# Optimization experiments

Hardware: AMD Instinct MI355X
Metric: run time of the kernel (lower is better)

The kernel has to match this reference:

```python
import jax, jax.numpy as jnp
import numpy as np

# Decode-mode paged attention: equivalent math to the Pallas paged_attention kernel
# the module dispatches to. Shapes per PagedAttentionOp init args.
B, H, D = 32, 32, 128        # decode batch, query heads, head dim
KVH = 8                      # num_kv_heads (GQA group = H // KVH = 4)
P, T = 2048, 64              # num_pages (global pool), tokens_per_page
PPS = 64                     # pages per sequence (page_map width)
MAXLEN = PPS * T             # 4096 max context


def setup_inputs() -> dict:
    key = jax.random.key(0)
    k1, k2, k3, k4, k5 = jax.random.split(key, 5)
    q = jax.random.normal(k1, (B, H, D), jnp.float32)
    k_pages = jax.random.normal(k2, (KVH, P, T, D), jnp.float32)
    v_pages = jax.random.normal(k3, (KVH, P, T, D), jnp.float32)
    lengths = jnp.maximum(jax.random.randint(k4, (B,), 0, MAXLEN), 1).astype(jnp.int32)
    page_indices = jax.random.randint(k5, (B, PPS), 0, P).astype(jnp.int32)
    return {"q": q, "k_pages": k_pages, "v_pages": v_pages,
            "lengths": lengths, "page_indices": page_indices}


def reference(q, k_pages, v_pages, lengths, page_indices):
    # q: [B, H, D]; k_pages/v_pages: [KVH, P, T, D]
    # lengths: [B] valid token counts; page_indices: [B, PPS] page table
    kvh, _, t, d = k_pages.shape
    b, h, _ = q.shape
    g = h // kvh                      # GQA group size
    s = page_indices.shape[1] * t     # gathered context length
    # page-table gather: [KVH, B, PPS, T, D] -> [KVH, B, S, D]
    k = jnp.take(k_pages, page_indices, axis=1).reshape(kvh, b, s, d)
    v = jnp.take(v_pages, page_indices, axis=1).reshape(kvh, b, s, d)
    qr = q.reshape(b, kvh, g, d)
    # no 1/sqrt(d) scaling: module never scales (MaxText pre-scales queries)
    scores = jnp.einsum('bkgd,kbsd->bkgs', qr, k)  # [B, KVH, G, S]
    valid = jnp.arange(s, dtype=jnp.int32)[None, :] < lengths[:, None]  # [B, S]
    scores = jnp.where(valid[:, None, None, :], scores, jnp.float32(-1e10))
    probs = jax.nn.softmax(scores, axis=-1)
    out = jnp.einsum('bkgs,kbsd->bkgd', probs, v)  # [B, KVH, G, D]
    return out.reshape(b, h, d)
```

## Files before the change

### kernel.cpp

```cpp
#include <hip/hip_runtime.h>
#include <math.h>

#define B_    32
#define H_    32
#define D_    128
#define KVH_  8
#define G_    4
#define P_    2048
#define T_    64
#define PPS_  64
#define NCHUNK 8
#define CHUNK_PAGES 8
#define RS4   33

__global__ __launch_bounds__(256, 2)
void pa_partial(const float* __restrict__ q,
                const float* __restrict__ k_pages,
                const float* __restrict__ v_pages,
                const int*   __restrict__ lengths,
                const int*   __restrict__ page_indices,
                float* __restrict__ o_part,
                float* __restrict__ m_part,
                float* __restrict__ l_part)
{
    __shared__ float4 K4[T_ * RS4];
    __shared__ float4 V4[T_ * RS4];
    __shared__ float4 q4s[G_ * 32];
    __shared__ float  p_s[G_ * T_];
    __shared__ float  alpha_s[G_];

    const int tid = threadIdx.x;
    const int bx  = blockIdx.x;
    const int c   = bx & (NCHUNK - 1);
    const int k   = (bx >> 3) & (KVH_ - 1);
    const int b   = bx >> 6;

    const int len = lengths[b];
    const int chunk_tok0 = c * (CHUNK_PAGES * T_);
    if (chunk_tok0 >= len) return;

    const int nP = (len + T_ - 1) / T_;
    const int p0 = c * CHUNK_PAGES;
    const int p1 = min(nP, p0 + CHUNK_PAGES);

    {
        const float* qg = q + ((size_t)b * H_ + (size_t)k * G_) * D_;
        ((float*)q4s)[tid]       = qg[tid];
        ((float*)q4s)[tid + 256] = qg[tid + 256];
    }

    const int g = tid >> 6;
    const int t = tid & 63;
    float m_run = -INFINITY;
    float l_run = 0.f;

    const int dq = tid & 31;
    const int th = tid >> 5;
    float4 oacc[G_];
#pragma unroll
    for (int i = 0; i < G_; ++i) { oacc[i].x = 0.f; oacc[i].y = 0.f; oacc[i].z = 0.f; oacc[i].w = 0.f; }

    __syncthreads();

    for (int p = p0; p < p1; ++p) {
        const int page = page_indices[b * PPS_ + p];
        const float4* Kg = (const float4*)(k_pages + ((size_t)k * P_ + (size_t)page) * (T_ * D_));
        const float4* Vg = (const float4*)(v_pages + ((size_t)k * P_ + (size_t)page) * (T_ * D_));

#pragma unroll
        for (int i = 0; i < 8; ++i) {
            const int f  = tid + 256 * i;
            const int tt = f >> 5;
            const int jj = f & 31;
            K4[tt * RS4 + jj] = Kg[f];
            V4[tt * RS4 + jj] = Vg[f];
        }
        __syncthreads();

        float s = 0.f;
        {
            const float4* Kr = &K4[t * RS4];
            const float4* qr = &q4s[g * 32];
#pragma unroll
            for (int i = 0; i < 32; ++i) {
                const float4 kv = Kr[i];
                const float4 qv = qr[i];
                s += kv.x * qv.x + kv.y * qv.y + kv.z * qv.z + kv.w * qv.w;
            }
        }
        const int tok = p * T_ + t;
        if (tok >= len) s = -1e30f;

        float smax = s;
#pragma unroll
        for (int off = 32; off; off >>= 1) smax = fmaxf(smax, __shfl_xor(smax, off));
        const float m_new = fmaxf(m_run, smax);
        const float pr    = __expf(s - m_new);
        const float alpha = __expf(m_run - m_new);
        float psum = pr;
#pragma unroll
        for (int off = 32; off; off >>= 1) psum += __shfl_xor(psum, off);
        l_run = alpha * l_run + psum;
        m_run = m_new;
        p_s[g * T_ + t] = pr;
        if (t == 0) alpha_s[g] = alpha;
        __syncthreads();

        const float a0 = alpha_s[0], a1 = alpha_s[1], a2 = alpha_s[2], a3 = alpha_s[3];
        oacc[0].x *= a0; oacc[0].y *= a0; oacc[0].z *= a0; oacc[0].w *= a0;
        oacc[1].x *= a1; oacc[1].y *= a1; oacc[1].z *= a1; oacc[1].w *= a1;
        oacc[2].x *= a2; oacc[2].y *= a2; oacc[2].z *= a2; oacc[2].w *= a2;
        oacc[3].x *= a3; oacc[3].y *= a3; oacc[3].z *= a3; oacc[3].w *= a3;
#pragma unroll
        for (int tt = 0; tt < 8; ++tt) {
            const int t2 = th * 8 + tt;
            const float4 vv = V4[t2 * RS4 + dq];
            const float pv0 = p_s[0 * T_ + t2];
            const float pv1 = p_s[1 * T_ + t2];
            const float pv2 = p_s[2 * T_ + t2];
            const float pv3 = p_s[3 * T_ + t2];
            oacc[0].x += pv0 * vv.x; oacc[0].y += pv0 * vv.y; oacc[0].z += pv0 * vv.z; oacc[0].w += pv0 * vv.w;
            oacc[1].x += pv1 * vv.x; oacc[1].y += pv1 * vv.y; oacc[1].z += pv1 * vv.z; oacc[1].w += pv1 * vv.w;
            oacc[2].x += pv2 * vv.x; oacc[2].y += pv2 * vv.y; oacc[2].z += pv2 * vv.z; oacc[2].w += pv2 * vv.w;
            oacc[3].x += pv3 * vv.x; oacc[3].y += pv3 * vv.y; oacc[3].z += pv3 * vv.z; oacc[3].w += pv3 * vv.w;
        }
        __syncthreads();
    }

    float4* red = K4;
#pragma unroll
    for (int g2 = 0; g2 < G_; ++g2) red[(th * G_ + g2) * 32 + dq] = oacc[g2];
    if (t == 0) { m_part[bx * G_ + g] = m_run; l_part[bx * G_ + g] = l_run; }
    __syncthreads();

    if (tid < 128) {
        const int gg = tid >> 5;
        const int dd = tid & 31;
        float4 sum; sum.x = 0.f; sum.y = 0.f; sum.z = 0.f; sum.w = 0.f;
#pragma unroll
        for (int th2 = 0; th2 < 8; ++th2) {
            const float4 v = red[(th2 * G_ + gg) * 32 + dd];
            sum.x += v.x; sum.y += v.y; sum.z += v.z; sum.w += v.w;
        }
        float4* op = (float4*)(o_part + (size_t)bx * (G_ * D_));
        op[gg * 32 + dd] = sum;
    }
}

__global__ __launch_bounds__(128)
void pa_reduce(const float* __restrict__ o_part,
               const float* __restrict__ m_part,
               const float* __restrict__ l_part,
               const int*   __restrict__ lengths,
               float* __restrict__ out)
{
    const int bx = blockIdx.x;
    const int gg = bx & 3;
    const int k  = (bx >> 2) & 7;
    const int b  = bx >> 5;
    const int len = lengths[b];
    const int nc  = (len + 511) >> 9;
    const int base = (b * KVH_ + k) * NCHUNK;

    float M = -INFINITY;
#pragma unroll
    for (int c = 0; c < NCHUNK; ++c)
        if (c < nc) M = fmaxf(M, m_part[(base + c) * G_ + gg]);

    const int d = threadIdx.x;
    float L = 0.f;
    float acc = 0.f;
#pragma unroll
    for (int c = 0; c < NCHUNK; ++c) {
        if (c < nc) {
            const float wc = __expf(m_part[(base + c) * G_ + gg] - M);
            L   += wc * l_part[(base + c) * G_ + gg];
            acc += wc * o_part[(size_t)(base + c) * (G_ * D_) + gg * D_ + d];
        }
    }
    out[((size_t)b * H_ + (size_t)k * G_ + gg) * D_ + d] = acc / L;
}

extern "C" void kernel_launch(void* const* d_in, const int* in_sizes, int n_in,
                              void* d_out, int out_size, void* d_ws, size_t ws_size,
                              hipStream_t stream) {
    const float* q            = (const float*)d_in[0];
    const float* k_pages      = (const float*)d_in[1];
    const float* v_pages      = (const float*)d_in[2];
    const int*   lengths      = (const int*)d_in[3];
    const int*   page_indices = (const int*)d_in[4];
    float* out = (float*)d_out;

    float* o_part = (float*)d_ws;
    float* m_part = o_part + (size_t)2048 * (G_ * D_);
    float* l_part = m_part + (size_t)2048 * G_;

    pa_partial<<<B_ * KVH_ * NCHUNK, 256, 0, stream>>>(
        q, k_pages, v_pages, lengths, page_indices, o_part, m_part, l_part);
    pa_reduce<<<B_ * KVH_ * G_, 128, 0, stream>>>(
        o_part, m_part, l_part, lengths, out);
}
```

Measured before the change: 922.0 us.

## Prefetch K pages via direct global-to-LDS loads, stream V through registers

K tiles are now staged asynchronously into LDS with global_load_lds and an XOR swizzle in place of padding, and the next page is prefetched while the current PV product runs. V is loaded straight into registers instead of going through shared memory, which halves LDS use and allows four blocks per CU. The split-K chunking doubles to 16 chunks of 4 pages for more parallelism, at the cost of more partial results to reduce. This relies on correct vmcnt handling at the barriers for the async LDS loads.

```diff
diff --git a/kernel.cpp b/kernel.cpp
--- a/kernel.cpp
+++ b/kernel.cpp
@@ -9,11 +9,16 @@
 #define P_    2048
 #define T_    64
 #define PPS_  64
-#define NCHUNK 8
-#define CHUNK_PAGES 8
-#define RS4   33
-
-__global__ __launch_bounds__(256, 2)
+#define NCHUNK 16
+#define CHUNK_PAGES 4
+
+__device__ __forceinline__ void load_lds16(const float4* g, void* l) {
+    __builtin_amdgcn_global_load_lds(
+        (const __attribute__((address_space(1))) void*)g,
+        (__attribute__((address_space(3))) void*)l, 16, 0, 0);
+}
+
+__global__ __launch_bounds__(256, 4)
 void pa_partial(const float* __restrict__ q,
                 const float* __restrict__ k_pages,
                 const float* __restrict__ v_pages,
@@ -23,8 +28,7 @@
                 float* __restrict__ m_part,
                 float* __restrict__ l_part)
 {
-    __shared__ float4 K4[T_ * RS4];
-    __shared__ float4 V4[T_ * RS4];
+    __shared__ float4 K4s[T_ * 32];
     __shared__ float4 q4s[G_ * 32];
     __shared__ float  p_s[G_ * T_];
     __shared__ float  alpha_s[G_];
@@ -32,14 +36,13 @@
     const int tid = threadIdx.x;
     const int bx  = blockIdx.x;
     const int c   = bx & (NCHUNK - 1);
-    const int k   = (bx >> 3) & (KVH_ - 1);
-    const int b   = bx >> 6;
+    const int k   = (bx >> 4) & (KVH_ - 1);
+    const int b   = bx >> 7;
 
     const int len = lengths[b];
-    const int chunk_tok0 = c * (CHUNK_PAGES * T_);
-    if (chunk_tok0 >= len) return;
-
-    const int nP = (len + T_ - 1) / T_;
+    if (c * (CHUNK_PAGES * T_) >= len) return;
+
+    const int nP = (len + T_ - 1) >> 6;
     const int p0 = c * CHUNK_PAGES;
     const int p1 = min(nP, p0 + CHUNK_PAGES);
 
@@ -49,46 +52,52 @@
         ((float*)q4s)[tid + 256] = qg[tid + 256];
     }
 
-    const int g = tid >> 6;
-    const int t = tid & 63;
+    const int g  = tid >> 6;
+    const int t  = tid & 63;
+    const int dq = tid & 31;
+    const int th = tid >> 5;
+
+    const int* pt = page_indices + b * PPS_;
+
     float m_run = -INFINITY;
     float l_run = 0.f;
-
-    const int dq = tid & 31;
-    const int th = tid >> 5;
     float4 oacc[G_];
 #pragma unroll
     for (int i = 0; i < G_; ++i) { oacc[i].x = 0.f; oacc[i].y = 0.f; oacc[i].z = 0.f; oacc[i].w = 0.f; }
 
-    __syncthreads();
+    auto stageK = [&](const float4* Kg) {
+#pragma unroll
+        for (int i = 0; i < 8; ++i) {
+            const int Lb = (g * 8 + i) * 64;
+            const int t_ = (Lb >> 5) + (t >> 5);
+            const int j_ = (t & 31) ^ (t_ & 7);
+            load_lds16(Kg + t_ * 32 + j_, (void*)&K4s[Lb]);
+        }
+    };
+
+    stageK((const float4*)(k_pages + ((size_t)k * P_ + pt[p0]) * (T_ * D_)));
 
     for (int p = p0; p < p1; ++p) {
-        const int page = page_indices[b * PPS_ + p];
-        const float4* Kg = (const float4*)(k_pages + ((size_t)k * P_ + (size_t)page) * (T_ * D_));
-        const float4* Vg = (const float4*)(v_pages + ((size_t)k * P_ + (size_t)page) * (T_ * D_));
-
-#pragma unroll
-        for (int i = 0; i < 8; ++i) {
-            const int f  = tid + 256 * i;
-            const int tt = f >> 5;
-            const int jj = f & 31;
-            K4[tt * RS4 + jj] = Kg[f];
-            V4[tt * RS4 + jj] = Vg[f];
-        }
         __syncthreads();
+
+        const float4* Vg = (const float4*)(v_pages + ((size_t)k * P_ + pt[p]) * (T_ * D_));
+        float4 vv[8];
+#pragma unroll
+        for (int tt = 0; tt < 8; ++tt) vv[tt] = Vg[(th * 8 + tt) * 32 + dq];
 
         float s = 0.f;
         {
-            const float4* Kr = &K4[t * RS4];
+            const float4* Kr = &K4s[t * 32];
             const float4* qr = &q4s[g * 32];
+            const int sw = t & 7;
 #pragma unroll
             for (int i = 0; i < 32; ++i) {
-                const float4 kv = Kr[i];
+                const float4 kv = Kr[i ^ sw];
                 const float4 qv = qr[i];
                 s += kv.x * qv.x + kv.y * qv.y + kv.z * qv.z + kv.w * qv.w;
             }
         }
-        const int tok = p * T_ + t;
+        const int tok = (p << 6) + t;
         if (tok >= len) s = -1e30f;
 
         float smax = s;
@@ -102,9 +111,12 @@
         for (int off = 32; off; off >>= 1) psum += __shfl_xor(psum, off);
         l_run = alpha * l_run + psum;
         m_run = m_new;
-        p_s[g * T_ + t] = pr;
+        p_s[(g << 6) + t] = pr;
         if (t == 0) alpha_s[g] = alpha;
         __syncthreads();
+
+        if (p + 1 < p1)
+            stageK((const float4*)(k_pages + ((size_t)k * P_ + pt[p + 1]) * (T_ * D_)));
 
         const float a0 = alpha_s[0], a1 = alpha_s[1], a2 = alpha_s[2], a3 = alpha_s[3];
         oacc[0].x *= a0; oacc[0].y *= a0; oacc[0].z *= a0; oacc[0].w *= a0;
@@ -113,21 +125,20 @@
         oacc[3].x *= a3; oacc[3].y *= a3; oacc[3].z *= a3; oacc[3].w *= a3;
 #pragma unroll
         for (int tt = 0; tt < 8; ++tt) {
-            const int t2 = th * 8 + tt;
-            const float4 vv = V4[t2 * RS4 + dq];
-            const float pv0 = p_s[0 * T_ + t2];
-            const float pv1 = p_s[1 * T_ + t2];
-            const float pv2 = p_s[2 * T_ + t2];
-            const float pv3 = p_s[3 * T_ + t2];
-            oacc[0].x += pv0 * vv.x; oacc[0].y += pv0 * vv.y; oacc[0].z += pv0 * vv.z; oacc[0].w += pv0 * vv.w;
-            oacc[1].x += pv1 * vv.x; oacc[1].y += pv1 * vv.y; oacc[1].z += pv1 * vv.z; oacc[1].w += pv1 * vv.w;
-            oacc[2].x += pv2 * vv.x; oacc[2].y += pv2 * vv.y; oacc[2].z += pv2 * vv.z; oacc[2].w += pv2 * vv.w;
-            oacc[3].x += pv3 * vv.x; oacc[3].y += pv3 * vv.y; oacc[3].z += pv3 * vv.z; oacc[3].w += pv3 * vv.w;
-        }
-        __syncthreads();
-    }
-
-    float4* red = K4;
+            const int t2 = (th << 3) + tt;
+            const float4 v4 = vv[tt];
+            const float pv0 = p_s[t2];
+            const float pv1 = p_s[64 + t2];
+            const float pv2 = p_s[128 + t2];
+            const float pv3 = p_s[192 + t2];
+            oacc[0].x += pv0 * v4.x; oacc[0].y += pv0 * v4.y; oacc[0].z += pv0 * v4.z; oacc[0].w += pv0 * v4.w;
+            oacc[1].x += pv1 * v4.x; oacc[1].y += pv1 * v4.y; oacc[1].z += pv1 * v4.z; oacc[1].w += pv1 * v4.w;
+            oacc[2].x += pv2 * v4.x; oacc[2].y += pv2 * v4.y; oacc[2].z += pv2 * v4.z; oacc[2].w += pv2 * v4.w;
+            oacc[3].x += pv3 * v4.x; oacc[3].y += pv3 * v4.y; oacc[3].z += pv3 * v4.z; oacc[3].w += pv3 * v4.w;
+        }
+    }
+
+    float4* red = K4s;
 #pragma unroll
     for (int g2 = 0; g2 < G_; ++g2) red[(th * G_ + g2) * 32 + dq] = oacc[g2];
     if (t == 0) { m_part[bx * G_ + g] = m_run; l_part[bx * G_ + g] = l_run; }
@@ -138,8 +149,8 @@
         const int dd = tid & 31;
         float4 sum; sum.x = 0.f; sum.y = 0.f; sum.z = 0.f; sum.w = 0.f;
 #pragma unroll
-        for (int th2 = 0; th2 < 8; ++th2) {
-            const float4 v = red[(th2 * G_ + gg) * 32 + dd];
+        for (int t8 = 0; t8 < 8; ++t8) {
+            const float4 v = red[(t8 * G_ + gg) * 32 + dd];
             sum.x += v.x; sum.y += v.y; sum.z += v.z; sum.w += v.w;
         }
         float4* op = (float4*)(o_part + (size_t)bx * (G_ * D_));
@@ -159,7 +170,7 @@
     const int k  = (bx >> 2) & 7;
     const int b  = bx >> 5;
     const int len = lengths[b];
-    const int nc  = (len + 511) >> 9;
+    const int nc  = (len + 255) >> 8;
     const int base = (b * KVH_ + k) * NCHUNK;
 
     float M = -INFINITY;
@@ -191,11 +202,12 @@
     const int*   page_indices = (const int*)d_in[4];
     float* out = (float*)d_out;
 
+    const int nblk = B_ * KVH_ * NCHUNK;
     float* o_part = (float*)d_ws;
-    float* m_part = o_part + (size_t)2048 * (G_ * D_);
-    float* l_part = m_part + (size_t)2048 * G_;
-
-    pa_partial<<<B_ * KVH_ * NCHUNK, 256, 0, stream>>>(
+    float* m_part = o_part + (size_t)nblk * (G_ * D_);
+    float* l_part = m_part + (size_t)nblk * G_;
+
+    pa_partial<<<nblk, 256, 0, stream>>>(
         q, k_pages, v_pages, lengths, page_indices, o_part, m_part, l_part);
     pa_reduce<<<B_ * KVH_ * G_, 128, 0, stream>>>(
         o_part, m_part, l_part, lengths, out);
```

Result: no change. 935.9 us (+1.5%).
